# Optimization experiments

Measured on AMD Instinct MI355X. Metric: run time of the kernel, lower is better.

## Reference

```python
import jax, jax.numpy as jnp
import numpy as np

N_HEAD = 16
HEAD_DIM = 64
EPS_RMS = 1e-6


def _rope(x, cos, sin):
    # x: [B, T, H, D]; cos/sin: [T, D//2] broadcast to [1, T, 1, D//2]
    d2 = x.shape[-1] // 2
    x1, x2 = x[..., :d2], x[..., d2:]
    c = cos[None, :, None, :]
    s = sin[None, :, None, :]
    return jnp.concatenate([x1 * c + x2 * s, -x1 * s + x2 * c], axis=-1)


def _rms_norm(x):
    return x * jax.lax.rsqrt(jnp.mean(x * x, axis=-1, keepdims=True) + EPS_RMS)


def setup_inputs() -> dict:
    key = jax.random.key(0)
    ks = jax.random.split(key, 7)
    B, T, C = 1, 4096, 1024
    x = jax.random.normal(ks[0], (B, T, C), dtype=jnp.float32)
    # realistic rotary angles
    d2 = HEAD_DIM // 2
    inv_freq = 1.0 / (10000.0 ** (np.arange(0, d2, dtype=np.float32) / d2))
    ang = np.arange(T, dtype=np.float32)[:, None] * inv_freq[None, :]
    cos = jnp.asarray(np.cos(ang), dtype=jnp.float32)
    sin = jnp.asarray(np.sin(ang), dtype=jnp.float32)
    scale = 0.02
    wq = jax.random.normal(ks[1], (C, C), dtype=jnp.float32) * scale
    wk = jax.random.normal(ks[2], (C, C), dtype=jnp.float32) * scale
    wv = jax.random.normal(ks[3], (C, C), dtype=jnp.float32) * scale
    wproj = jax.random.normal(ks[4], (C, C), dtype=jnp.float32) * scale
    return {"x": x, "cos": cos, "sin": sin, "wq": wq, "wk": wk, "wv": wv, "wproj": wproj}


def reference(x, cos, sin, wq, wk, wv, wproj):
    B, T, C = x.shape
    H, D = N_HEAD, HEAD_DIM
    # QKV projections (torch Linear: x @ W.T)
    q = (x @ wq.T).reshape(B, T, H, D)
    k = (x @ wk.T).reshape(B, T, H, D)
    v = (x @ wv.T).reshape(B, T, H, D)
    # RoPE then QK RMS-norm
    q = _rms_norm(_rope(q, cos, sin))
    k = _rms_norm(_rope(k, cos, sin))
    # [B, H, T, D]
    q = q.transpose(0, 2, 1, 3)
    k = k.transpose(0, 2, 1, 3)
    v = v.transpose(0, 2, 1, 3)
    scores = jnp.einsum('bhqd,bhkd->bhqk', q, k) * (1.0 / D ** 0.5)
    # causal mask (kv_cache is None, Tq == Tk == T)
    mask = jnp.tril(jnp.ones((T, T), dtype=bool))
    scores = jnp.where(mask[None, None, :, :], scores, -jnp.inf)
    attn = jax.nn.sigmoid(scores)  # sigmoid(-inf) == 0
    y = jnp.einsum('bhqk,bhkd->bhqd', attn, v)
    y = y / (T ** 0.5 + 1e-6)
    y = y.transpose(0, 2, 1, 3).reshape(B, T, C)
    return y @ wproj.T
```

## Files before the change

kernel.cpp:

```cpp
#include <hip/hip_runtime.h>

typedef __attribute__((ext_vector_type(8))) short bf16x8;
typedef __attribute__((ext_vector_type(4))) float f32x4;
typedef __attribute__((ext_vector_type(16))) float f32x16;

__device__ inline f32x4 mfma16(bf16x8 a, bf16x8 b, f32x4 c) {
    return __builtin_amdgcn_mfma_f32_16x16x32_bf16(a, b, c, 0, 0, 0);
}
__device__ inline f32x16 mfma32(bf16x8 a, bf16x8 b, f32x16 c) {
    return __builtin_amdgcn_mfma_f32_32x32x16_bf16(a, b, c, 0, 0, 0);
}

__device__ inline short f2bf(float f) {
    unsigned u = __builtin_bit_cast(unsigned, f);
    unsigned r = (u + 0x7fffu + ((u >> 16) & 1u)) >> 16;
    return (short)r;
}
__device__ inline float bf2f(short h) {
    unsigned u = ((unsigned)(unsigned short)h) << 16;
    return __builtin_bit_cast(float, u);
}

__device__ inline unsigned cvt_pk_bf16(float lo, float hi) {
    unsigned r;
    asm("v_cvt_pk_bf16_f32 %0, %1, %2" : "=v"(r) : "v"(lo), "v"(hi));
    return r;
}
__device__ inline void plane_swap(unsigned& a, unsigned& b) {
    asm("v_permlane32_swap_b32 %0, %1" : "+v"(a), "+v"(b));
}
__device__ inline float exp2_hw(float x) {
    float r;
    asm("v_exp_f32 %0, %1" : "=v"(r) : "v"(x));
    return r;
}

#define GAS(p) (const __attribute__((address_space(1))) void*)(p)
#define LAS(p) (__attribute__((address_space(3))) void*)(p)

#define T_SEQ 4096
#define C_DIM 1024
#define N_HEAD 16
#define HEAD_DIM 64
#define QSCALE (-0.18033688011112042f)
#define INV64 (1.0f / (64.0f + 1e-6f))

__global__ __launch_bounds__(256) void cast5(
    const float* __restrict__ s0, const float* __restrict__ s1,
    const float* __restrict__ s2, const float* __restrict__ s3,
    const float* __restrict__ s4,
    short* __restrict__ d0, short* __restrict__ d1, short* __restrict__ d2,
    short* __restrict__ d3, short* __restrict__ d4,
    int n0, int n1, int n2, int n3, int n4)
{
    int z = blockIdx.y;
    const float* s; short* d; int n;
    switch (z) {
        case 0: s = s0; d = d0; n = n0; break;
        case 1: s = s1; d = d1; n = n1; break;
        case 2: s = s2; d = d2; n = n2; break;
        case 3: s = s3; d = d3; n = n3; break;
        default: s = s4; d = d4; n = n4; break;
    }
    float sc = (z == 4) ? INV64 : 1.0f;
    int i = (blockIdx.x * 256 + threadIdx.x) * 4;
    if (i >= n) return;
    float4 v = *(const float4*)&s[i];
    short4 o;
    o.x = f2bf(v.x * sc); o.y = f2bf(v.y * sc);
    o.z = f2bf(v.z * sc); o.w = f2bf(v.w * sc);
    *(short4*)&d[i] = o;
}

#define QSTAGE(t_, b_) do {                                                      \
    int k0_ = (t_) * 32;                                                         \
    _Pragma("unroll")                                                            \
    for (int s2_ = 0; s2_ < 2; s2_++) {                                          \
        int rbase_ = wave * 32 + s2_ * 16;                                       \
        __builtin_amdgcn_global_load_lds(                                        \
            GAS(&A[(size_t)(row0 + rbase_ + srow) * KK + k0_ + scolx]),          \
            LAS(&sA[b_][rbase_ * 32]), 16, 0, 0);                                \
        __builtin_amdgcn_global_load_lds(                                        \
            GAS(&B[(size_t)(col0 + rbase_ + srow) * KK + k0_ + scolx]),          \
            LAS(&sB[b_][rbase_ * 32]), 16, 0, 0);                                \
    }                                                                            \
} while (0)

#define GEMM_STEP2(t_, nt_, bcur_) do {                                          \
    if ((t_) + 1 < (nt_)) {                                                      \
        QSTAGE((t_) + 1, (bcur_) ^ 1);                                           \
        asm volatile("s_waitcnt vmcnt(4)" ::: "memory");                         \
    } else {                                                                     \
        asm volatile("s_waitcnt vmcnt(0)" ::: "memory");                         \
    }                                                                            \
    __builtin_amdgcn_s_barrier();                                                \
    bf16x8 af[4], bfv[4];                                                        \
    _Pragma("unroll")                                                            \
    for (int m = 0; m < 4; m++) {                                                \
        int row_ = wr * 64 + m * 16 + llo;                                       \
        af[m] = *(const bf16x8*)&sA[bcur_][row_ * 32 + ((lhi ^ (llo & 3)) * 8)]; \
    }                                                                            \
    _Pragma("unroll")                                                            \
    for (int n = 0; n < 4; n++) {                                                \
        int row_ = wc * 64 + n * 16 + llo;                                       \
        bfv[n] = *(const bf16x8*)&sB[bcur_][row_ * 32 + ((lhi ^ (llo & 3)) * 8)];\
    }                                                                            \
    __builtin_amdgcn_s_setprio(1);                                               \
    _Pragma("unroll")                                                            \
    for (int m = 0; m < 4; m++)                                                  \
        _Pragma("unroll")                                                        \
        for (int n = 0; n < 4; n++)                                              \
            acc[m][n] = mfma16(af[m], bfv[n], acc[m][n]);                        \
    __builtin_amdgcn_s_setprio(0);                                               \
    asm volatile("" ::: "memory");                                               \
    __builtin_amdgcn_s_barrier();                                                \
} while (0)

__global__ __launch_bounds__(256, 4) void gemm_qkv(
    const short* __restrict__ A,
    const short* __restrict__ B0, const short* __restrict__ B1,
    const short* __restrict__ B2,
    short* __restrict__ qnb, short* __restrict__ knb, short* __restrict__ vnb,
    const float* __restrict__ cosT, const float* __restrict__ sinT)
{
    int xx = blockIdx.x;
    int ct = xx & 7, z = xx >> 3;
    const short* B = (z == 0) ? B0 : ((z == 1) ? B1 : B2);
    short* dst     = (z == 0) ? qnb : ((z == 1) ? knb : vnb);

    __shared__ alignas(16) short sA[2][128 * 32];
    __shared__ alignas(16) short sB[2][128 * 32];

    int tid  = threadIdx.x;
    int wave = tid >> 6, lane = tid & 63;
    int lhi  = lane >> 4, llo = lane & 15;
    int wr   = wave >> 1, wc = wave & 1;
    int row0 = blockIdx.y * 128, col0 = ct * 128;
    const int KK = C_DIM;

    int srow  = lane >> 2;
    int scolx = (((lane & 3) ^ (srow & 3)) * 8);

    f32x4 acc[4][4];
#pragma unroll
    for (int m = 0; m < 4; m++)
#pragma unroll
        for (int n = 0; n < 4; n++)
            acc[m][n] = (f32x4){0.f, 0.f, 0.f, 0.f};

    QSTAGE(0, 0);
    int bcur = 0;
    for (int t = 0; t < 32; t++) {
        GEMM_STEP2(t, 32, bcur);
        bcur ^= 1;
    }

    int hH = ct * 2 + wc;
    if (z < 2) {
        float osc = z ? 1.0f : QSCALE;
#pragma unroll
        for (int m = 0; m < 4; m++)
#pragma unroll
            for (int r = 0; r < 4; r++) {
                int row = row0 + wr * 64 + m * 16 + lhi * 4 + r;
                float c0 = cosT[row * 32 + llo],      c1 = cosT[row * 32 + 16 + llo];
                float s0 = sinT[row * 32 + llo],      s1 = sinT[row * 32 + 16 + llo];
                float e0 = acc[m][0][r], e1 = acc[m][1][r];
                float e2 = acc[m][2][r], e3 = acc[m][3][r];
                float r0 = e0 * c0 + e2 * s0;
                float r1 = e1 * c1 + e3 * s1;
                float r2 = e2 * c0 - e0 * s0;
                float r3 = e3 * c1 - e1 * s1;
                float sq = r0 * r0 + r1 * r1 + r2 * r2 + r3 * r3;
                sq += __shfl_xor(sq, 1);
                sq += __shfl_xor(sq, 2);
                sq += __shfl_xor(sq, 4);
                sq += __shfl_xor(sq, 8);
                float inv = rsqrtf(sq * (1.0f / 64.0f) + 1e-6f) * osc;
                size_t base = ((size_t)hH * T_SEQ + row) * HEAD_DIM + llo;
                dst[base +  0] = f2bf(r0 * inv);
                dst[base + 16] = f2bf(r1 * inv);
                dst[base + 32] = f2bf(r2 * inv);
                dst[base + 48] = f2bf(r3 * inv);
            }
    } else {
#pragma unroll
        for (int m = 0; m < 4; m++)
#pragma unroll
            for (int r = 0; r < 4; r++) {
                int row = row0 + wr * 64 + m * 16 + lhi * 4 + r;
                size_t base = ((size_t)hH * T_SEQ + row) * HEAD_DIM + llo;
#pragma unroll
                for (int n = 0; n < 4; n++)
                    dst[base + n * 16] = f2bf(acc[m][n][r]);
            }
    }
}

__global__ __launch_bounds__(256, 4) void gemm_proj(
    const short* __restrict__ A, const short* __restrict__ B,
    float* __restrict__ C, int M, int N, int K)
{
    __shared__ alignas(16) short sA[2][128 * 32];
    __shared__ alignas(16) short sB[2][128 * 32];

    int tid  = threadIdx.x;
    int wave = tid >> 6, lane = tid & 63;
    int lhi  = lane >> 4, llo = lane & 15;
    int wr   = wave >> 1, wc = wave & 1;
    int row0 = blockIdx.y * 128, col0 = blockIdx.x * 128;
    const int KK = K;

    int srow  = lane >> 2;
    int scolx = (((lane & 3) ^ (srow & 3)) * 8);

    f32x4 acc[4][4];
#pragma unroll
    for (int m = 0; m < 4; m++)
#pragma unroll
        for (int n = 0; n < 4; n++)
            acc[m][n] = (f32x4){0.f, 0.f, 0.f, 0.f};

    int nt = K >> 5;
    QSTAGE(0, 0);
    int bcur = 0;
    for (int t = 0; t < nt; t++) {
        GEMM_STEP2(t, nt, bcur);
        bcur ^= 1;
    }

#pragma unroll
    for (int m = 0; m < 4; m++)
#pragma unroll
        for (int n = 0; n < 4; n++)
#pragma unroll
            for (int r = 0; r < 4; r++) {
                int row = row0 + wr * 64 + m * 16 + lhi * 4 + r;
                int col = col0 + wc * 64 + n * 16 + llo;
                C[(size_t)row * N + col] = acc[m][n][r];
            }
}

__global__ __launch_bounds__(256) void vtrans(
    const short* __restrict__ vnb, short* __restrict__ vt)
{
    __shared__ short sT[64 * 72];
    int h = blockIdx.y, tb = blockIdx.x;
    int tid = threadIdx.x;
#pragma unroll
    for (int p = 0; p < 2; p++) {
        int r  = p * 32 + (tid >> 3);
        int c0 = (tid & 7) * 8;
        bf16x8 v = *(const bf16x8*)&vnb[((size_t)h * T_SEQ + tb * 64 + r) * HEAD_DIM + c0];
#pragma unroll
        for (int j = 0; j < 8; j++) sT[(c0 + j) * 72 + r] = v[j];
    }
    __syncthreads();
#pragma unroll
    for (int p = 0; p < 2; p++) {
        int dd = p * 32 + (tid >> 3);
        int t0 = (tid & 7) * 8;
        bf16x8 o = *(const bf16x8*)&sT[dd * 72 + t0];
        *(bf16x8*)&vt[((size_t)(h * HEAD_DIM + dd)) * T_SEQ + tb * 64 + t0] = o;
    }
}

#define STAGE6(s_, bf_) do {                                                     \
    int kb_ = (s_) * 64;                                                         \
    int r_  = lane >> 3;                                                         \
    int ss_ = (lane & 7) ^ r_;                                                   \
    __builtin_amdgcn_global_load_lds(                                            \
        GAS(Kh + (size_t)(kb_ + wv * 16 + r_) * HEAD_DIM + ss_ * 8),             \
        LAS(Smem + (bf_) * 8192 + (wv * 16) * 128), 16, 0, 0);                   \
    __builtin_amdgcn_global_load_lds(                                            \
        GAS(Kh + (size_t)(kb_ + wv * 16 + 8 + r_) * HEAD_DIM + ss_ * 8),         \
        LAS(Smem + (bf_) * 8192 + (wv * 16 + 8) * 128), 16, 0, 0);               \
    __builtin_amdgcn_global_load_lds(                                            \
        GAS(Vh + (size_t)(wv * 16 + r_) * T_SEQ + kb_ + ss_ * 8),                \
        LAS(Smem + 16384 + (bf_) * 8192 + (wv * 16) * 128), 16, 0, 0);           \
    __builtin_amdgcn_global_load_lds(                                            \
        GAS(Vh + (size_t)(wv * 16 + 8 + r_) * T_SEQ + kb_ + ss_ * 8),            \
        LAS(Smem + 16384 + (bf_) * 8192 + (wv * 16 + 8) * 128), 16, 0, 0);       \
} while (0)

__global__ __launch_bounds__(256, 4) void attn6(
    const short* __restrict__ qn, const short* __restrict__ kn,
    const short* __restrict__ vt, short* __restrict__ yb)
{
    __shared__ alignas(16) char Smem[32768];

    int id = blockIdx.x;
    int h  = id & 15;
    int g  = id >> 4;
    int t  = (g < 16) ? (63 - g) : (g < 32) ? (g - 16)
           : (g < 48) ? (79 - g) : (g - 32);
    int ns = t + 1;

    int tid = threadIdx.x, wv = tid >> 6, lane = tid & 63;
    int lo = lane & 31, hi = lane >> 5;
    int band = wv & 1, tm = wv >> 1;

    const short* Qh = qn + (size_t)h * T_SEQ * HEAD_DIM;
    const short* Kh = kn + (size_t)h * T_SEQ * HEAD_DIM;
    const short* Vh = vt + (size_t)h * HEAD_DIM * T_SEQ;

    int q0 = t * 64;
    int qrow  = q0 + band * 32 + lo;
    int qmaxw = q0 + band * 32 + 31;

    const short* Qr = &Qh[(size_t)qrow * HEAD_DIM + hi * 8];
    bf16x8 qf0 = *(const bf16x8*)&Qr[0];
    bf16x8 qf1 = *(const bf16x8*)&Qr[16];
    bf16x8 qf2 = *(const bf16x8*)&Qr[32];
    bf16x8 qf3 = *(const bf16x8*)&Qr[48];

    f32x16 zed;
#pragma unroll
    for (int r = 0; r < 16; r++) zed[r] = 0.f;

    f32x16 yac0, yac1;
#pragma unroll
    for (int r = 0; r < 16; r++) { yac0[r] = 0.f; yac1[r] = 0.f; }

    unsigned sw   = (unsigned)((lo & 7) << 4);
    unsigned krow = (unsigned)((tm * 32 + lo) * 128);
    unsigned ko0 = krow + ((0u * 32 + hi * 16) ^ sw);
    unsigned ko1 = krow + ((1u * 32 + hi * 16) ^ sw);
    unsigned ko2 = krow + ((2u * 32 + hi * 16) ^ sw);
    unsigned ko3 = krow + ((3u * 32 + hi * 16) ^ sw);
    unsigned vrow0 = (unsigned)(lo * 128)        + 16384u;
    unsigned vrow1 = (unsigned)((32 + lo) * 128) + 16384u;
    unsigned vo00 = vrow0 + (((unsigned)(tm * 64 + 0 * 32 + hi * 16)) ^ sw);
    unsigned vo01 = vrow0 + (((unsigned)(tm * 64 + 1 * 32 + hi * 16)) ^ sw);
    unsigned vo10 = vrow1 + (((unsigned)(tm * 64 + 0 * 32 + hi * 16)) ^ sw);
    unsigned vo11 = vrow1 + (((unsigned)(tm * 64 + 1 * 32 + hi * 16)) ^ sw);

    STAGE6(0, 0);
    int buf = 0;
    for (int s = 0; s < ns; s++) {
        if (s + 1 < ns) {
            STAGE6(s + 1, buf ^ 1);
            asm volatile("s_waitcnt vmcnt(4)" ::: "memory");
        } else {
            asm volatile("s_waitcnt vmcnt(0)" ::: "memory");
        }
        __builtin_amdgcn_s_barrier();

        int kb0 = s * 64 + tm * 32;
        if (kb0 <= qmaxw) {
            const char* B_ = Smem + (buf << 13);
            bf16x8 kf0 = *(const bf16x8*)(B_ + ko0);
            bf16x8 kf1 = *(const bf16x8*)(B_ + ko1);
            bf16x8 kf2 = *(const bf16x8*)(B_ + ko2);
            bf16x8 kf3 = *(const bf16x8*)(B_ + ko3);
            bf16x8 vf00 = *(const bf16x8*)(B_ + vo00);
            bf16x8 vf01 = *(const bf16x8*)(B_ + vo01);
            bf16x8 vf10 = *(const bf16x8*)(B_ + vo10);
            bf16x8 vf11 = *(const bf16x8*)(B_ + vo11);

            f32x16 sv;
            __builtin_amdgcn_s_setprio(1);
            sv = mfma32(kf0, qf0, zed);
            sv = mfma32(kf1, qf1, sv);
            sv = mfma32(kf2, qf2, sv);
            sv = mfma32(kf3, qf3, sv);
            __builtin_amdgcn_s_setprio(0);

            if (kb0 + 31 > q0 + band * 32) {
#pragma unroll
                for (int r = 0; r < 16; r++) {
                    int kvg = kb0 + (r & 3) + 8 * (r >> 2) + 4 * hi;
                    float pv = __builtin_amdgcn_rcpf(1.f + exp2_hw(sv[r]));
                    sv[r] = (kvg <= qrow) ? pv : 0.f;
                }
            } else {
#pragma unroll
                for (int r = 0; r < 16; r++)
                    sv[r] = __builtin_amdgcn_rcpf(1.f + exp2_hw(sv[r]));
            }

#pragma unroll
            for (int k2 = 0; k2 < 2; k2++) {
                unsigned wA = cvt_pk_bf16(sv[8 * k2 + 0], sv[8 * k2 + 1]);
                unsigned wC = cvt_pk_bf16(sv[8 * k2 + 2], sv[8 * k2 + 3]);
                unsigned wB = cvt_pk_bf16(sv[8 * k2 + 4], sv[8 * k2 + 5]);
                unsigned wD = cvt_pk_bf16(sv[8 * k2 + 6], sv[8 * k2 + 7]);
                plane_swap(wA, wB);
                plane_swap(wC, wD);
                union { unsigned u[4]; bf16x8 v; } pw;
                pw.u[0] = wA; pw.u[1] = wC; pw.u[2] = wB; pw.u[3] = wD;
                __builtin_amdgcn_s_setprio(1);
                yac0 = mfma32(pw.v, k2 ? vf01 : vf00, yac0);
                yac1 = mfma32(pw.v, k2 ? vf11 : vf10, yac1);
                __builtin_amdgcn_s_setprio(0);
            }
        }
        asm volatile("" ::: "memory");
        __builtin_amdgcn_s_barrier();
        buf ^= 1;
    }

    __syncthreads();
    float* Yred = (float*)Smem;
    if (tm == 1) {
#pragma unroll
        for (int d = 0; d < 2; d++)
#pragma unroll
            for (int r = 0; r < 16; r++) {
                int crow = (r & 3) + 8 * (r >> 2) + 4 * hi;
                Yred[(band * 32 + crow) * 64 + d * 32 + lo] = d ? yac1[r] : yac0[r];
            }
    }
    __syncthreads();
    if (tm == 0) {
#pragma unroll
        for (int d = 0; d < 2; d++)
#pragma unroll
            for (int r = 0; r < 16; r++) {
                int crow = (r & 3) + 8 * (r >> 2) + 4 * hi;
                float v = (d ? yac1[r] : yac0[r]) + Yred[(band * 32 + crow) * 64 + d * 32 + lo];
                yb[(size_t)(q0 + band * 32 + crow) * C_DIM + h * HEAD_DIM + d * 32 + lo] = f2bf(v);
            }
    }
}

extern "C" void kernel_launch(void* const* d_in, const int* in_sizes, int n_in,
                              void* d_out, int out_size, void* d_ws, size_t ws_size,
                              hipStream_t stream)
{
    const float* x    = (const float*)d_in[0];
    const float* cosT = (const float*)d_in[1];
    const float* sinT = (const float*)d_in[2];
    const float* wq   = (const float*)d_in[3];
    const float* wk   = (const float*)d_in[4];
    const float* wv   = (const float*)d_in[5];
    const float* wp   = (const float*)d_in[6];

    char* ws = (char*)d_ws;
    const size_t MB = 1024 * 1024;
    short* xb    = (short*)(ws + 0);
    short* wqb   = (short*)(ws + 8  * MB);
    short* wkb   = (short*)(ws + 10 * MB);
    short* wvb   = (short*)(ws + 12 * MB);
    short* wpb   = (short*)(ws + 14 * MB);
    short* qnb   = (short*)(ws + 16 * MB);
    short* knb   = (short*)(ws + 24 * MB);
    short* vnb   = (short*)(ws + 32 * MB);
    short* vtb   = (short*)(ws + 40 * MB);
    short* yb    = (short*)(ws + 48 * MB);

    cast5<<<dim3(4096, 5, 1), 256, 0, stream>>>(
        x, wq, wk, wv, wp, xb, wqb, wkb, wvb, wpb,
        T_SEQ * C_DIM, C_DIM * C_DIM, C_DIM * C_DIM, C_DIM * C_DIM, C_DIM * C_DIM);

    gemm_qkv<<<dim3(24, 32, 1), 256, 0, stream>>>(
        xb, wqb, wkb, wvb, qnb, knb, vnb, cosT, sinT);

    vtrans<<<dim3(64, 16, 1), 256, 0, stream>>>(vnb, vtb);

    attn6<<<1024, 256, 0, stream>>>(qnb, knb, vtb, yb);

    gemm_proj<<<dim3(8, 32, 1), 256, 0, stream>>>(
        yb, wpb, (float*)d_out, T_SEQ, C_DIM, C_DIM);
}
```

Measured before the change: 133.4 us.

## Software-pipeline attention loop: overlap next tile's QK MFMA with current sigmoid

Restructures the causal sigmoid-attention main loop so that the QK^T MFMAs for tile s+1 are issued after the sigmoid and bf16 packing of tile s, and before the PV MFMAs of tile s. The loop is manually unrolled by two with ping-pong score registers and LDS buffers, and exits via a goto on the last tile. The aim is to overlap transcendental VALU work with matrix-core work. In exchange, the wait for the next tile's global-to-LDS load now comes right after it is issued, so it overlaps only the sigmoid phase. The per-wave skip of fully masked key tiles is also dropped, which adds some wasted MFMAs on diagonal tiles.

```diff
diff --git a/kernel.cpp b/kernel.cpp
--- a/kernel.cpp
+++ b/kernel.cpp
@@ -265,6 +265,7 @@
     }
 }
 
+
 #define STAGE6(s_, bf_) do {                                                     \
     int kb_ = (s_) * 64;                                                         \
     int r_  = lane >> 3;                                                         \
@@ -283,7 +284,71 @@
         LAS(Smem + 16384 + (bf_) * 8192 + (wv * 16 + 8) * 128), 16, 0, 0);       \
 } while (0)
 
-__global__ __launch_bounds__(256, 4) void attn6(
+#define PSTEP(svc_, svn_, cbo_, nbo_, bi_) {                                     \
+    int last_ = (s + 1 >= ns);                                                   \
+    if (!last_) STAGE6(s + 1, bi_);                                              \
+                                            \
+    int kb0_ = s * 64 + tm * 32;                                                 \
+    if (kb0_ + 31 > qminw) {                                                     \
+        _Pragma("unroll") for (int r = 0; r < 16; r++) {                         \
+            int kvg_ = kb0_ + (r & 3) + 8 * (r >> 2) + 4 * hi;                   \
+            float pv_ = __builtin_amdgcn_rcpf(1.f + exp2_hw(svc_[r]));           \
+            svc_[r] = (kvg_ <= qrow) ? pv_ : 0.f;                                \
+        }                                                                        \
+    } else {                                                                     \
+        _Pragma("unroll") for (int r = 0; r < 16; r++)                           \
+            svc_[r] = __builtin_amdgcn_rcpf(1.f + exp2_hw(svc_[r]));             \
+    }                                                                            \
+    union { unsigned u[4]; bf16x8 v; } pw0_, pw1_;                               \
+    {                                                                            \
+        unsigned a_ = cvt_pk_bf16(svc_[0], svc_[1]);                             \
+        unsigned c_ = cvt_pk_bf16(svc_[2], svc_[3]);                             \
+        unsigned b_ = cvt_pk_bf16(svc_[4], svc_[5]);                             \
+        unsigned d_ = cvt_pk_bf16(svc_[6], svc_[7]);                             \
+        plane_swap(a_, b_); plane_swap(c_, d_);                                  \
+        pw0_.u[0] = a_; pw0_.u[1] = c_; pw0_.u[2] = b_; pw0_.u[3] = d_;          \
+        unsigned e_ = cvt_pk_bf16(svc_[8],  svc_[9]);                            \
+        unsigned g_ = cvt_pk_bf16(svc_[10], svc_[11]);                           \
+        unsigned f_ = cvt_pk_bf16(svc_[12], svc_[13]);                           \
+        unsigned h_ = cvt_pk_bf16(svc_[14], svc_[15]);                           \
+        plane_swap(e_, f_); plane_swap(g_, h_);                                  \
+        pw1_.u[0] = e_; pw1_.u[1] = g_; pw1_.u[2] = f_; pw1_.u[3] = h_;          \
+    }                                                                            \
+    if (!last_) {                                                                \
+        asm volatile("s_waitcnt vmcnt(0)" ::: "memory");                         \
+        __builtin_amdgcn_s_barrier();                                            \
+        const char* NB_ = Smem + (nbo_);                                         \
+        bf16x8 kf0_ = *(const bf16x8*)(NB_ + ko0);                               \
+        bf16x8 kf1_ = *(const bf16x8*)(NB_ + ko1);                               \
+        bf16x8 kf2_ = *(const bf16x8*)(NB_ + ko2);                               \
+        bf16x8 kf3_ = *(const bf16x8*)(NB_ + ko3);                               \
+        __builtin_amdgcn_s_setprio(1);                                           \
+        svn_ = mfma32(kf0_, qf0, zed);                                           \
+        svn_ = mfma32(kf1_, qf1, svn_);                                          \
+        svn_ = mfma32(kf2_, qf2, svn_);                                          \
+        svn_ = mfma32(kf3_, qf3, svn_);                                          \
+        __builtin_amdgcn_s_setprio(0);                                           \
+    }                                                                            \
+    const char* CB_ = Smem + (cbo_);                                             \
+    bf16x8 vf00_ = *(const bf16x8*)(CB_ + vo00);                                 \
+    bf16x8 vf01_ = *(const bf16x8*)(CB_ + vo01);                                 \
+    bf16x8 vf10_ = *(const bf16x8*)(CB_ + vo10);                                 \
+    bf16x8 vf11_ = *(const bf16x8*)(CB_ + vo11);                                 \
+    __builtin_amdgcn_s_setprio(1);                                               \
+    yac0 = mfma32(pw0_.v, vf00_, yac0);                                          \
+    yac1 = mfma32(pw0_.v, vf10_, yac1);                                          \
+    yac0 = mfma32(pw1_.v, vf01_, yac0);                                          \
+    yac1 = mfma32(pw1_.v, vf11_, yac1);                                          \
+    __builtin_amdgcn_s_setprio(0);                                               \
+    if (last_) goto eplg;                                                        \
+        \
+               \
+    asm volatile("" ::: "memory");                                               \
+    __builtin_amdgcn_s_barrier();                                                \
+    s++;                                                                         \
+}
+
+__global__ __launch_bounds__(256, 4) void attn15(
     const short* __restrict__ qn, const short* __restrict__ kn,
     const short* __restrict__ vt, short* __restrict__ yb)
 {
@@ -306,7 +371,7 @@
 
     int q0 = t * 64;
     int qrow  = q0 + band * 32 + lo;
-    int qmaxw = q0 + band * 32 + 31;
+    int qminw = q0 + band * 32;
 
     const short* Qr = &Qh[(size_t)qrow * HEAD_DIM + hi * 8];
     bf16x8 qf0 = *(const bf16x8*)&Qr[0];
@@ -336,69 +401,31 @@
     unsigned vo11 = vrow1 + (((unsigned)(tm * 64 + 1 * 32 + hi * 16)) ^ sw);
 
     STAGE6(0, 0);
-    int buf = 0;
-    for (int s = 0; s < ns; s++) {
-        if (s + 1 < ns) {
-            STAGE6(s + 1, buf ^ 1);
-            asm volatile("s_waitcnt vmcnt(4)" ::: "memory");
-        } else {
-            asm volatile("s_waitcnt vmcnt(0)" ::: "memory");
+    asm volatile("s_waitcnt vmcnt(0)" ::: "memory");
+    __builtin_amdgcn_s_barrier();
+
+    f32x16 svA, svB;
+    {
+        bf16x8 kf0 = *(const bf16x8*)(Smem + ko0);
+        bf16x8 kf1 = *(const bf16x8*)(Smem + ko1);
+        bf16x8 kf2 = *(const bf16x8*)(Smem + ko2);
+        bf16x8 kf3 = *(const bf16x8*)(Smem + ko3);
+        __builtin_amdgcn_s_setprio(1);
+        svA = mfma32(kf0, qf0, zed);
+        svA = mfma32(kf1, qf1, svA);
+        svA = mfma32(kf2, qf2, svA);
+        svA = mfma32(kf3, qf3, svA);
+        __builtin_amdgcn_s_setprio(0);
+    }
+
+    {
+        int s = 0;
+        while (true) {
+            PSTEP(svA, svB, 0, 8192, 1);
+            PSTEP(svB, svA, 8192, 0, 0);
         }
-        __builtin_amdgcn_s_barrier();
-
-        int kb0 = s * 64 + tm * 32;
-        if (kb0 <= qmaxw) {
-            const char* B_ = Smem + (buf << 13);
-            bf16x8 kf0 = *(const bf16x8*)(B_ + ko0);
-            bf16x8 kf1 = *(const bf16x8*)(B_ + ko1);
-            bf16x8 kf2 = *(const bf16x8*)(B_ + ko2);
-            bf16x8 kf3 = *(const bf16x8*)(B_ + ko3);
-            bf16x8 vf00 = *(const bf16x8*)(B_ + vo00);
-            bf16x8 vf01 = *(const bf16x8*)(B_ + vo01);
-            bf16x8 vf10 = *(const bf16x8*)(B_ + vo10);
-            bf16x8 vf11 = *(const bf16x8*)(B_ + vo11);
-
-            f32x16 sv;
-            __builtin_amdgcn_s_setprio(1);
-            sv = mfma32(kf0, qf0, zed);
-            sv = mfma32(kf1, qf1, sv);
-            sv = mfma32(kf2, qf2, sv);
-            sv = mfma32(kf3, qf3, sv);
-            __builtin_amdgcn_s_setprio(0);
-
-            if (kb0 + 31 > q0 + band * 32) {
-#pragma unroll
-                for (int r = 0; r < 16; r++) {
-                    int kvg = kb0 + (r & 3) + 8 * (r >> 2) + 4 * hi;
-                    float pv = __builtin_amdgcn_rcpf(1.f + exp2_hw(sv[r]));
-                    sv[r] = (kvg <= qrow) ? pv : 0.f;
-                }
-            } else {
-#pragma unroll
-                for (int r = 0; r < 16; r++)
-                    sv[r] = __builtin_amdgcn_rcpf(1.f + exp2_hw(sv[r]));
-            }
-
-#pragma unroll
-            for (int k2 = 0; k2 < 2; k2++) {
-                unsigned wA = cvt_pk_bf16(sv[8 * k2 + 0], sv[8 * k2 + 1]);
-                unsigned wC = cvt_pk_bf16(sv[8 * k2 + 2], sv[8 * k2 + 3]);
-                unsigned wB = cvt_pk_bf16(sv[8 * k2 + 4], sv[8 * k2 + 5]);
-                unsigned wD = cvt_pk_bf16(sv[8 * k2 + 6], sv[8 * k2 + 7]);
-                plane_swap(wA, wB);
-                plane_swap(wC, wD);
-                union { unsigned u[4]; bf16x8 v; } pw;
-                pw.u[0] = wA; pw.u[1] = wC; pw.u[2] = wB; pw.u[3] = wD;
-                __builtin_amdgcn_s_setprio(1);
-                yac0 = mfma32(pw.v, k2 ? vf01 : vf00, yac0);
-                yac1 = mfma32(pw.v, k2 ? vf11 : vf10, yac1);
-                __builtin_amdgcn_s_setprio(0);
-            }
-        }
-        asm volatile("" ::: "memory");
-        __builtin_amdgcn_s_barrier();
-        buf ^= 1;
-    }
+    }
+eplg:
 
     __syncthreads();
     float* Yred = (float*)Smem;
@@ -458,7 +485,7 @@
 
     vtrans<<<dim3(64, 16, 1), 256, 0, stream>>>(vnb, vtb);
 
-    attn6<<<1024, 256, 0, stream>>>(qnb, knb, vtb, yb);
+    attn15<<<1024, 256, 0, stream>>>(qnb, knb, vtb, yb);
 
     gemm_proj<<<dim3(8, 32, 1), 256, 0, stream>>>(
         yb, wpb, (float*)d_out, T_SEQ, C_DIM, C_DIM);
```

Measured after the change: 142.3 us. 1.07x slower.
